# Kernel optimization log

Measured on AMD Instinct MI355X. Metric: run time of the kernel, lower is better.

The kernel has to match this reference:

```python
import jax, jax.numpy as jnp
import numpy as np

NUM_HEADS = 32
NUM_KV_HEADS = 8
HEAD_DIM = 128
ROPE_THETA = 10000.0


def _rope_cos_sin(seq_len, head_dim, dtype):
    # [seq, head_dim/2] angles, duplicated to [seq, head_dim] via concat (rotate-half convention)
    inv_freq = 1.0 / (ROPE_THETA ** (jnp.arange(0, head_dim, 2, dtype=jnp.float32) / head_dim))
    ang = jnp.arange(seq_len, dtype=jnp.float32)[:, None] * inv_freq[None, :]
    ang = jnp.concatenate([ang, ang], axis=-1)
    return jnp.cos(ang).astype(dtype), jnp.sin(ang).astype(dtype)


def _rotate_half(x):
    d = x.shape[-1] // 2
    return jnp.concatenate([-x[..., d:], x[..., :d]], axis=-1)


def setup_inputs() -> dict:
    key = jax.random.key(0)
    ks = jax.random.split(key, 5)
    E = NUM_HEADS * HEAD_DIM
    KVE = NUM_KV_HEADS * HEAD_DIM
    B, S = 2, 2048
    sc_in = 1.0 / np.sqrt(E)
    return {
        "x": jax.random.normal(ks[0], (B, S, E), jnp.float32),
        "Wq": jax.random.normal(ks[1], (E, E), jnp.float32) * sc_in,
        "Wk": jax.random.normal(ks[2], (E, KVE), jnp.float32) * sc_in,
        "Wv": jax.random.normal(ks[3], (E, KVE), jnp.float32) * sc_in,
        "Wo": jax.random.normal(ks[4], (E, E), jnp.float32) * sc_in,
    }


def reference(x, Wq, Wk, Wv, Wo):
    b, s, e = x.shape
    H, KV, D = NUM_HEADS, NUM_KV_HEADS, HEAD_DIM
    G = H // KV
    scale = 1.0 / np.sqrt(D)

    q = (x @ Wq).reshape(b, s, H, D).transpose(0, 2, 1, 3)    # [b,H,s,D]
    k = (x @ Wk).reshape(b, s, KV, D).transpose(0, 2, 1, 3)   # [b,KV,s,D]
    v = (x @ Wv).reshape(b, s, KV, D).transpose(0, 2, 1, 3)   # [b,KV,s,D]

    cos, sin = _rope_cos_sin(s, D, q.dtype)                   # [s,D]
    q = q * cos + _rotate_half(q) * sin
    k = k * cos + _rotate_half(k) * sin

    # GQA: group q heads by kv head instead of repeat_interleaving k/v
    qg = q.reshape(b, KV, G, s, D)
    attn = jnp.einsum("bkgqd,bkvd->bkgqv", qg, k) * scale     # [b,KV,G,s,s]

    causal = jnp.where(
        jnp.arange(s)[:, None] >= jnp.arange(s)[None, :], 0.0, -jnp.inf
    ).astype(jnp.float32)
    attn = attn.astype(jnp.float32) + causal
    attn = jax.nn.softmax(attn, axis=-1).astype(q.dtype)

    out = jnp.einsum("bkgqv,bkvd->bkgqd", attn, v)            # [b,KV,G,s,D]
    out = out.reshape(b, H, s, D).transpose(0, 2, 1, 3).reshape(b, s, H * D)
    return out @ Wo
```

## Files before the change

kernel.cpp:

```cpp
#include <hip/hip_runtime.h>
#include <stdint.h>
#include <math.h>

typedef short bf16x8 __attribute__((ext_vector_type(8)));
typedef float f32x4 __attribute__((ext_vector_type(4)));

#if __has_builtin(__builtin_amdgcn_exp2f)
#define EXP2F(x) __builtin_amdgcn_exp2f(x)
#else
#define EXP2F(x) exp2f(x)
#endif

static constexpr int Bn   = 2;
static constexpr int Sn   = 2048;
static constexpr int NH   = 32;
static constexpr int NKV  = 8;
static constexpr int Dh   = 128;
static constexpr int En   = NH * Dh;
static constexpr int KVEn = NKV * Dh;
static constexpr int QKVE = En + 2 * KVEn;
static constexpr int MT   = Bn * Sn;
static constexpr int QT   = Sn / 128;

__device__ __forceinline__ unsigned short f2bf(float f) {
  unsigned int u = __float_as_uint(f);
  u += 0x7FFFu + ((u >> 16) & 1u);
  return (unsigned short)(u >> 16);
}
__device__ __forceinline__ float bf2f(unsigned short h) {
  return __uint_as_float(((unsigned int)h) << 16);
}

typedef __attribute__((address_space(1))) void* gas_t;
typedef __attribute__((address_space(3))) void* las_t;
__device__ __forceinline__ void gl_lds16(const void* g, void* l) {
  __builtin_amdgcn_global_load_lds((gas_t)(uintptr_t)g, (las_t)(uint32_t)(uintptr_t)l,
                                   16, 0, 0);
}


__global__ void cast_bf16_kernel(const float* __restrict__ x,
                                 unsigned short* __restrict__ y, int n4) {
  int i = blockIdx.x * 256 + threadIdx.x;
  if (i >= n4) return;
  float4 v = ((const float4*)x)[i];
  ushort4 o;
  o.x = f2bf(v.x); o.y = f2bf(v.y); o.z = f2bf(v.z); o.w = f2bf(v.w);
  ((ushort4*)y)[i] = o;
}

__global__ void tcast_kernel(const float* __restrict__ W,
                             unsigned short* __restrict__ WT, int R, int C) {
  __shared__ float t[32][33];
  int tx = threadIdx.x, ty = threadIdx.y;
  int c = blockIdx.x * 32 + tx, r = blockIdx.y * 32 + ty;
  t[ty][tx] = W[(size_t)r * C + c];
  __syncthreads();
  int ro = blockIdx.x * 32 + ty, co = blockIdx.y * 32 + tx;
  WT[(size_t)ro * R + co] = f2bf(t[tx][ty]);
}

__global__ void rope_table_kernel(float2* __restrict__ cs) {
  int i = blockIdx.x * 256 + threadIdx.x;
  int s = i >> 6, d = i & 63;
  float inv = powf(10000.0f, -(float)d * (1.0f / 64.0f));
  float a = (float)s * inv;
  cs[i] = make_float2(cosf(a), sinf(a));
}

__global__ void rope_kernel(unsigned short* __restrict__ q,
                            const float2* __restrict__ cs, int rowstride, float scl) {
  int row = blockIdx.x;
  int s = row & (Sn - 1);
  int hl = threadIdx.x >> 6, d = threadIdx.x & 63;
  int h = blockIdx.y * 4 + hl;
  size_t base = (size_t)row * rowstride + (size_t)h * Dh + d;
  float2 c = cs[s * 64 + d];
  float x0 = bf2f(q[base]), x1 = bf2f(q[base + 64]);
  q[base]      = f2bf((x0 * c.x - x1 * c.y) * scl);
  q[base + 64] = f2bf((x1 * c.x + x0 * c.y) * scl);
}

__global__ void vtrans_kernel(const unsigned short* __restrict__ V, int rowstride,
                              unsigned short* __restrict__ Vt) {
  __shared__ unsigned short t[32][33];
  int bk = blockIdx.z;
  int b = bk >> 3, kv = bk & 7;
  int d = blockIdx.x * 32 + threadIdx.x;
  int s = blockIdx.y * 32 + threadIdx.y;
  t[threadIdx.y][threadIdx.x] = V[(size_t)(b * Sn + s) * rowstride + kv * Dh + d];
  __syncthreads();
  int dd = blockIdx.x * 32 + threadIdx.y;
  int so = blockIdx.y * 32 + threadIdx.x;
  Vt[((size_t)bk * Dh + dd) * Sn + so] = t[threadIdx.x][threadIdx.y];
}


__global__ __launch_bounds__(512, 2) void gemm256_kernel(
    const unsigned short* __restrict__ A, const unsigned short* __restrict__ BT,
    void* __restrict__ Cout, int M, int N, int K, int out_f32) {
  __shared__ unsigned short lds[2][4][128 * 64];
  const int tid = threadIdx.x;
  const int lane = tid & 63, wave = tid >> 6;
  const int r15 = lane & 15, kg = lane >> 4;
  const int wm = wave >> 2, wn = wave & 3;
  const int m0 = blockIdx.y * 256, n0 = blockIdx.x * 256;
  const char* Ab = (const char*)A;
  const char* Bb = (const char*)BT;
  const int KT = K >> 6;

  f32x4 acc[8][4] = {};

  auto stage = [&](int ktile, int buf) {
    int k0 = ktile * 64;
#pragma unroll
    for (int half = 0; half < 2; ++half)
#pragma unroll
      for (int ld = 0; ld < 2; ++ld) {
        int f = (ld * 512 + tid) * 16;
        int row = f >> 7, cb = f & 127;
        int scb = cb ^ ((row & 7) << 4);
        gl_lds16(Ab + ((size_t)(m0 + half * 128 + row) * K + k0) * 2 + scb,
                 (char*)lds[buf][half] + f);
        gl_lds16(Bb + ((size_t)(n0 + half * 128 + row) * K + k0) * 2 + scb,
                 (char*)lds[buf][2 + half] + f);
      }
  };

  stage(0, 0);
  stage(1, 1);
  asm volatile("s_waitcnt vmcnt(8)" ::: "memory");
  __builtin_amdgcn_sched_barrier(0);
  __builtin_amdgcn_s_barrier();
  __builtin_amdgcn_sched_barrier(0);

  for (int kt = 0; kt < KT; ++kt) {
    const int cur = kt & 1;
    const char* Abase = (const char*)lds[cur][wm];
    const char* Bbase = (const char*)lds[cur][2 + (wn >> 1)];
    const int brow0 = (wn & 1) * 64;

#pragma unroll
    for (int ks = 0; ks < 2; ++ks) {
      bf16x8 bfr[4];
#pragma unroll
      for (int nf = 0; nf < 4; ++nf) {
        int br = brow0 + nf * 16 + r15;
        bfr[nf] = *(const bf16x8*)(Bbase + br * 128 +
                                   ((ks * 64 + kg * 16) ^ ((br & 7) << 4)));
      }
#pragma unroll
      for (int mh = 0; mh < 2; ++mh) {
        bf16x8 afr[4];
#pragma unroll
        for (int mf = 0; mf < 4; ++mf) {
          int ar = mh * 64 + mf * 16 + r15;
          afr[mf] = *(const bf16x8*)(Abase + ar * 128 +
                                     ((ks * 64 + kg * 16) ^ ((ar & 7) << 4)));
        }
        __builtin_amdgcn_s_setprio(1);
#pragma unroll
        for (int mf = 0; mf < 4; ++mf)
#pragma unroll
          for (int nf = 0; nf < 4; ++nf)
            acc[mh * 4 + mf][nf] = __builtin_amdgcn_mfma_f32_16x16x32_bf16(
                afr[mf], bfr[nf], acc[mh * 4 + mf][nf], 0, 0, 0);
        __builtin_amdgcn_s_setprio(0);
      }
    }

    __builtin_amdgcn_sched_barrier(0);
    __builtin_amdgcn_s_barrier();
    __builtin_amdgcn_sched_barrier(0);
    if (kt + 2 < KT) {
      stage(kt + 2, cur);
      asm volatile("s_waitcnt vmcnt(8)" ::: "memory");
    } else {
      asm volatile("s_waitcnt vmcnt(0)" ::: "memory");
    }
    __builtin_amdgcn_sched_barrier(0);
    __builtin_amdgcn_s_barrier();
    __builtin_amdgcn_sched_barrier(0);
  }

#pragma unroll
  for (int mh = 0; mh < 2; ++mh)
#pragma unroll
    for (int mf = 0; mf < 4; ++mf)
#pragma unroll
      for (int nf = 0; nf < 4; ++nf)
#pragma unroll
        for (int t = 0; t < 4; ++t) {
          int row = m0 + wm * 128 + mh * 64 + mf * 16 + kg * 4 + t;
          int col = n0 + wn * 64 + nf * 16 + r15;
          if (out_f32)
            ((float*)Cout)[(size_t)row * N + col] = acc[mh * 4 + mf][nf][t];
          else
            ((unsigned short*)Cout)[(size_t)row * N + col] = f2bf(acc[mh * 4 + mf][nf][t]);
        }
}


__device__ __forceinline__ void sm_update(f32x4 sc[4], f32x4 o[8],
                                          float mrow[4], float lrow[4],
                                          bool diag, int qrow0, int kt,
                                          int r15, int kg, char* Pw) {
  if (diag) {
#pragma unroll
    for (int kf = 0; kf < 4; ++kf) {
      int kvg = kt * 64 + kf * 16 + r15;
#pragma unroll
      for (int t = 0; t < 4; ++t)
        if (kvg > qrow0 + kg * 4 + t) sc[kf][t] = -1e30f;
    }
  }
  float mx[4], sm[4];
#pragma unroll
  for (int t = 0; t < 4; ++t) {
    float v = fmaxf(fmaxf(sc[0][t], sc[1][t]), fmaxf(sc[2][t], sc[3][t]));
#pragma unroll
    for (int off = 1; off < 16; off <<= 1) v = fmaxf(v, __shfl_xor(v, off, 16));
    mx[t] = fmaxf(mrow[t], v);
    sm[t] = EXP2F(mrow[t] - mx[t]);
    mrow[t] = mx[t];
  }
#pragma unroll
  for (int kf = 0; kf < 4; ++kf)
#pragma unroll
    for (int t = 0; t < 4; ++t) sc[kf][t] = EXP2F(sc[kf][t] - mx[t]);
#pragma unroll
  for (int t = 0; t < 4; ++t) {
    float v = sc[0][t] + sc[1][t] + sc[2][t] + sc[3][t];
#pragma unroll
    for (int off = 1; off < 16; off <<= 1) v += __shfl_xor(v, off, 16);
    lrow[t] = lrow[t] * sm[t] + v;
  }
#pragma unroll
  for (int nf = 0; nf < 8; ++nf)
#pragma unroll
    for (int t = 0; t < 4; ++t) o[nf][t] *= sm[t];
#pragma unroll
  for (int kf = 0; kf < 4; ++kf)
#pragma unroll
    for (int t = 0; t < 4; ++t) {
      int r = kg * 4 + t, c = kf * 16 + r15;
      *(unsigned short*)(Pw + r * 128 + ((c * 2) ^ ((r & 7) << 4))) = f2bf(sc[kf][t]);
    }
}

__global__ __launch_bounds__(512, 4) void attn_kernel(
    const unsigned short* __restrict__ Q, const unsigned short* __restrict__ Kl,
    const unsigned short* __restrict__ Vt, unsigned short* __restrict__ AO) {
  __shared__ unsigned short Ks[2][64 * 128];
  __shared__ unsigned short Vs[2][128 * 64];
  __shared__ unsigned short Ps[8][16 * 64];
  const int tid = threadIdx.x, lane = tid & 63, wave = tid >> 6;
  const int h = blockIdx.x, b = blockIdx.z;
  const int qt = (QT - 1) - blockIdx.y;
  const int kvh = h >> 2;
  const int r15 = lane & 15, kg = lane >> 4;
  const int qrow0 = qt * 128 + wave * 16;
  const int kmax = 2 * qt + 2;

  bf16x8 qf[4];
#pragma unroll
  for (int db = 0; db < 4; ++db)
    qf[db] = *(const bf16x8*)&Q[(size_t)(b * Sn + qrow0 + r15) * QKVE +
                                h * Dh + db * 32 + kg * 8];

  f32x4 o[8] = {};
  float mrow[4] = {-1e30f, -1e30f, -1e30f, -1e30f};
  float lrow[4] = {0.f, 0.f, 0.f, 0.f};

  const char* Kbase = (const char*)Kl + (size_t)(b * Sn) * (QKVE * 2) + kvh * 256;
  const char* Vbase = (const char*)Vt + (size_t)((b * NKV + kvh) * Dh) * (Sn * 2);

  auto stage = [&](int kt, int bi) {
#pragma unroll
    for (int c = 0; c < 2; ++c) {
      int f = (c * 512 + tid) * 16;
      int row = f >> 8, cb = f & 255;
      gl_lds16(Kbase + (size_t)(kt * 64 + row) * (QKVE * 2) + (cb ^ ((row & 7) << 4)),
               (char*)Ks[bi] + f);
    }
#pragma unroll
    for (int c = 0; c < 2; ++c) {
      int f = (c * 512 + tid) * 16;
      int row = f >> 7, cb = f & 127;
      gl_lds16(Vbase + (size_t)row * (Sn * 2) + kt * 128 + (cb ^ ((row & 7) << 4)),
               (char*)Vs[bi] + f);
    }
  };

  stage(0, 0);
  __syncthreads();

  for (int kt = 0; kt < kmax; ++kt) {
    const int cur = kt & 1;
    if (kt + 1 < kmax) stage(kt + 1, cur ^ 1);
    if (kt * 64 <= qrow0 + 15) {
      const char* Kc = (const char*)Ks[cur];
      const char* Vc = (const char*)Vs[cur];
      f32x4 sc[4] = {};
      __builtin_amdgcn_s_setprio(1);
#pragma unroll
      for (int db = 0; db < 4; ++db) {
#pragma unroll
        for (int kf = 0; kf < 4; ++kf) {
          int krow = kf * 16 + r15;
          int cb = (db * 32 + kg * 8) * 2;
          bf16x8 kb = *(const bf16x8*)(Kc + krow * 256 + (cb ^ ((krow & 7) << 4)));
          sc[kf] = __builtin_amdgcn_mfma_f32_16x16x32_bf16(qf[db], kb, sc[kf], 0, 0, 0);
        }
      }
      __builtin_amdgcn_s_setprio(0);

      char* Pw = (char*)Ps[wave];
      bool diag = (kt * 64 + 63) > qrow0;
      sm_update(sc, o, mrow, lrow, diag, qrow0, kt, r15, kg, Pw);

      __builtin_amdgcn_s_setprio(1);
#pragma unroll
      for (int ks = 0; ks < 2; ++ks) {
        bf16x8 pa = *(const bf16x8*)(Pw + r15 * 128 + ((kg * 16 + ks * 64) ^ ((r15 & 7) << 4)));
#pragma unroll
        for (int nf = 0; nf < 8; ++nf) {
          int vrow = nf * 16 + r15;
          int cb = (ks * 32 + kg * 8) * 2;
          bf16x8 vb = *(const bf16x8*)(Vc + vrow * 128 + (cb ^ ((vrow & 7) << 4)));
          o[nf] = __builtin_amdgcn_mfma_f32_16x16x32_bf16(pa, vb, o[nf], 0, 0, 0);
        }
      }
      __builtin_amdgcn_s_setprio(0);
    }
    __syncthreads();
  }

  float rinv[4];
#pragma unroll
  for (int t = 0; t < 4; ++t) rinv[t] = 1.0f / lrow[t];
#pragma unroll
  for (int nf = 0; nf < 8; ++nf)
#pragma unroll
    for (int t = 0; t < 4; ++t) {
      int srow = qrow0 + kg * 4 + t;
      AO[(size_t)(b * Sn + srow) * En + h * Dh + nf * 16 + r15] = f2bf(o[nf][t] * rinv[t]);
    }
}


extern "C" void kernel_launch(void* const* d_in, const int* in_sizes, int n_in,
                              void* d_out, int out_size, void* d_ws, size_t ws_size,
                              hipStream_t stream) {
  const float* x  = (const float*)d_in[0];
  const float* Wq = (const float*)d_in[1];
  const float* Wk = (const float*)d_in[2];
  const float* Wv = (const float*)d_in[3];
  const float* Wo = (const float*)d_in[4];

  char* ws = (char*)d_ws;
  size_t off = 0;
  auto alloc = [&](size_t bytes) -> char* {
    char* p = ws + off;
    off += (bytes + 255) & ~(size_t)255;
    return p;
  };
  unsigned short* xb   = (unsigned short*)alloc((size_t)MT * En * 2);
  unsigned short* Wqkv = (unsigned short*)alloc((size_t)QKVE * En * 2);
  unsigned short* WoT  = (unsigned short*)alloc((size_t)En * En * 2);
  unsigned short* Cqkv = (unsigned short*)alloc((size_t)MT * QKVE * 2);
  unsigned short* Vt   = (unsigned short*)alloc((size_t)MT * KVEn * 2);
  float2* cs           = (float2*)alloc((size_t)Sn * 64 * sizeof(float2));
  unsigned short* AO   = xb;

  cast_bf16_kernel<<<MT * (En / 4) / 256, 256, 0, stream>>>(x, xb, MT * En / 4);
  tcast_kernel<<<dim3(En / 32, En / 32), dim3(32, 32), 0, stream>>>(Wq, Wqkv, En, En);
  tcast_kernel<<<dim3(KVEn / 32, En / 32), dim3(32, 32), 0, stream>>>(
      Wk, Wqkv + (size_t)En * En, En, KVEn);
  tcast_kernel<<<dim3(KVEn / 32, En / 32), dim3(32, 32), 0, stream>>>(
      Wv, Wqkv + (size_t)(En + KVEn) * En, En, KVEn);
  tcast_kernel<<<dim3(En / 32, En / 32), dim3(32, 32), 0, stream>>>(Wo, WoT, En, En);
  rope_table_kernel<<<Sn * 64 / 256, 256, 0, stream>>>(cs);

  gemm256_kernel<<<dim3(QKVE / 256, MT / 256), 512, 0, stream>>>(
      xb, Wqkv, Cqkv, MT, QKVE, En, 0);

  const float scl = 0.08838834764831845f * 1.4426950408889634f;
  rope_kernel<<<dim3(MT, NH / 4), 256, 0, stream>>>(Cqkv, cs, QKVE, scl);
  rope_kernel<<<dim3(MT, NKV / 4), 256, 0, stream>>>(Cqkv + En, cs, QKVE, 1.0f);
  vtrans_kernel<<<dim3(Dh / 32, Sn / 32, Bn * NKV), dim3(32, 32), 0, stream>>>(
      Cqkv + En + KVEn, QKVE, Vt);

  attn_kernel<<<dim3(NH, QT, Bn), 512, 0, stream>>>(Cqkv, Cqkv + En, Vt, AO);

  gemm256_kernel<<<dim3(En / 256, MT / 256), 512, 0, stream>>>(
      AO, WoT, d_out, MT, En, En, 1);
}
```

Baseline: 619.8 us.

## Restructure bf16 GEMM into 8-phase ping-pong schedule with per-quadrant staging

Rewrites the 256x256 GEMM main loop as eight phases per pair of K-tiles. Each phase computes one 128x128 quadrant (mh, nh) and issues the global-to-LDS load of one half-tile, so that loads and MFMA work are interleaved at finer granularity. The warp-to-output mapping changes from a 2x4 layout with 128x64 per wave to 64x32 sub-blocks repeated in each quadrant, and A and B fragments are reused across phases. This adds more barriers and hand-tuned vmcnt waits, and it assumes KT is even and at least 4.

```diff
diff --git a/kernel.cpp b/kernel.cpp
--- a/kernel.cpp
+++ b/kernel.cpp
@@ -37,6 +37,11 @@
   __builtin_amdgcn_global_load_lds((gas_t)(uintptr_t)g, (las_t)(uint32_t)(uintptr_t)l,
                                    16, 0, 0);
 }
+
+#define VMW(n)  asm volatile("s_waitcnt vmcnt(" #n ")" ::: "memory")
+#define LGKM0   asm volatile("s_waitcnt lgkmcnt(0)" ::: "memory")
+#define SCHEDB  __builtin_amdgcn_sched_barrier(0)
+#define BAR     __builtin_amdgcn_s_barrier()
 
 
 __global__ void cast_bf16_kernel(const float* __restrict__ x,
@@ -103,101 +108,119 @@
   const int tid = threadIdx.x;
   const int lane = tid & 63, wave = tid >> 6;
   const int r15 = lane & 15, kg = lane >> 4;
-  const int wm = wave >> 2, wn = wave & 3;
+  const int wr = wave >> 2, wc = wave & 3;
   const int m0 = blockIdx.y * 256, n0 = blockIdx.x * 256;
   const char* Ab = (const char*)A;
   const char* Bb = (const char*)BT;
   const int KT = K >> 6;
 
-  f32x4 acc[8][4] = {};
-
-  auto stage = [&](int ktile, int buf) {
-    int k0 = ktile * 64;
-#pragma unroll
-    for (int half = 0; half < 2; ++half)
-#pragma unroll
-      for (int ld = 0; ld < 2; ++ld) {
-        int f = (ld * 512 + tid) * 16;
-        int row = f >> 7, cb = f & 127;
-        int scb = cb ^ ((row & 7) << 4);
-        gl_lds16(Ab + ((size_t)(m0 + half * 128 + row) * K + k0) * 2 + scb,
-                 (char*)lds[buf][half] + f);
-        gl_lds16(Bb + ((size_t)(n0 + half * 128 + row) * K + k0) * 2 + scb,
-                 (char*)lds[buf][2 + half] + f);
-      }
-  };
-
-  stage(0, 0);
-  stage(1, 1);
-  asm volatile("s_waitcnt vmcnt(8)" ::: "memory");
-  __builtin_amdgcn_sched_barrier(0);
-  __builtin_amdgcn_s_barrier();
-  __builtin_amdgcn_sched_barrier(0);
-
-  for (int kt = 0; kt < KT; ++kt) {
-    const int cur = kt & 1;
-    const char* Abase = (const char*)lds[cur][wm];
-    const char* Bbase = (const char*)lds[cur][2 + (wn >> 1)];
-    const int brow0 = (wn & 1) * 64;
-
-#pragma unroll
-    for (int ks = 0; ks < 2; ++ks) {
-      bf16x8 bfr[4];
-#pragma unroll
-      for (int nf = 0; nf < 4; ++nf) {
-        int br = brow0 + nf * 16 + r15;
-        bfr[nf] = *(const bf16x8*)(Bbase + br * 128 +
-                                   ((ks * 64 + kg * 16) ^ ((br & 7) << 4)));
-      }
-#pragma unroll
-      for (int mh = 0; mh < 2; ++mh) {
-        bf16x8 afr[4];
-#pragma unroll
-        for (int mf = 0; mf < 4; ++mf) {
-          int ar = mh * 64 + mf * 16 + r15;
-          afr[mf] = *(const bf16x8*)(Abase + ar * 128 +
-                                     ((ks * 64 + kg * 16) ^ ((ar & 7) << 4)));
-        }
-        __builtin_amdgcn_s_setprio(1);
-#pragma unroll
-        for (int mf = 0; mf < 4; ++mf)
-#pragma unroll
-          for (int nf = 0; nf < 4; ++nf)
-            acc[mh * 4 + mf][nf] = __builtin_amdgcn_mfma_f32_16x16x32_bf16(
-                afr[mf], bfr[nf], acc[mh * 4 + mf][nf], 0, 0, 0);
-        __builtin_amdgcn_s_setprio(0);
-      }
-    }
-
-    __builtin_amdgcn_sched_barrier(0);
-    __builtin_amdgcn_s_barrier();
-    __builtin_amdgcn_sched_barrier(0);
-    if (kt + 2 < KT) {
-      stage(kt + 2, cur);
-      asm volatile("s_waitcnt vmcnt(8)" ::: "memory");
-    } else {
-      asm volatile("s_waitcnt vmcnt(0)" ::: "memory");
-    }
-    __builtin_amdgcn_sched_barrier(0);
-    __builtin_amdgcn_s_barrier();
-    __builtin_amdgcn_sched_barrier(0);
+  f32x4 acc[2][2][4][2] = {};
+  bf16x8 ar[4][2];
+  bf16x8 br[2][2][2];
+
+#define STAGE_H(SRC, ROW0, KT_, SLOT)                                         \
+  do {                                                                        \
+    _Pragma("unroll") for (int ld = 0; ld < 2; ++ld) {                        \
+      int _f = (ld * 512 + tid) * 16;                                         \
+      int _row = _f >> 7, _cb = _f & 127;                                     \
+      gl_lds16(SRC + ((size_t)((ROW0) + _row) * K + (KT_) * 64) * 2 +         \
+                   (_cb ^ ((_row & 7) << 4)),                                 \
+               (char*)(SLOT) + _f);                                           \
+    }                                                                         \
+  } while (0)
+
+#define GPHASE(MH, NH, BUF, DO_LDA, DO_LDB, STAGE_STMT, WAIT_STMT)            \
+  do {                                                                        \
+    if (DO_LDA) {                                                             \
+      const char* _as = (const char*)lds[BUF][MH];                            \
+      _Pragma("unroll") for (int mf = 0; mf < 4; ++mf) {                      \
+        int _r = wr * 64 + mf * 16 + r15;                                     \
+        int _sw = (_r & 7) << 4;                                              \
+        ar[mf][0] = *(const bf16x8*)(_as + _r * 128 + ((kg * 16) ^ _sw));     \
+        ar[mf][1] = *(const bf16x8*)(_as + _r * 128 + ((64 + kg * 16) ^ _sw));\
+      }                                                                       \
+    }                                                                         \
+    if (DO_LDB) {                                                             \
+      const char* _bs = (const char*)lds[BUF][2 + NH];                        \
+      _Pragma("unroll") for (int nf = 0; nf < 2; ++nf) {                      \
+        int _r = wc * 32 + nf * 16 + r15;                                     \
+        int _sw = (_r & 7) << 4;                                              \
+        br[NH][nf][0] =                                                       \
+            *(const bf16x8*)(_bs + _r * 128 + ((kg * 16) ^ _sw));             \
+        br[NH][nf][1] =                                                       \
+            *(const bf16x8*)(_bs + _r * 128 + ((64 + kg * 16) ^ _sw));        \
+      }                                                                       \
+    }                                                                         \
+    STAGE_STMT;                                                               \
+    BAR;                                                                      \
+    if ((DO_LDA) || (DO_LDB)) { LGKM0; }                                      \
+    SCHEDB;                                                                   \
+    __builtin_amdgcn_s_setprio(1);                                            \
+    _Pragma("unroll") for (int mf = 0; mf < 4; ++mf)                          \
+      _Pragma("unroll") for (int nf = 0; nf < 2; ++nf) {                      \
+        acc[MH][NH][mf][nf] = __builtin_amdgcn_mfma_f32_16x16x32_bf16(        \
+            ar[mf][0], br[NH][nf][0], acc[MH][NH][mf][nf], 0, 0, 0);          \
+        acc[MH][NH][mf][nf] = __builtin_amdgcn_mfma_f32_16x16x32_bf16(        \
+            ar[mf][1], br[NH][nf][1], acc[MH][NH][mf][nf], 0, 0, 0);          \
+      }                                                                       \
+    __builtin_amdgcn_s_setprio(0);                                            \
+    SCHEDB;                                                                   \
+    WAIT_STMT;                                                                \
+    BAR;                                                                      \
+    SCHEDB;                                                                   \
+  } while (0)
+
+  STAGE_H(Ab, m0,       0, lds[0][0]);
+  STAGE_H(Bb, n0,       0, lds[0][2]);
+  STAGE_H(Ab, m0 + 128, 0, lds[0][1]);
+  STAGE_H(Bb, n0 + 128, 0, lds[0][3]);
+  STAGE_H(Ab, m0,       1, lds[1][0]);
+  STAGE_H(Bb, n0,       1, lds[1][2]);
+  VMW(8);
+  SCHEDB;
+  BAR;
+  SCHEDB;
+
+  for (int k = 0; k + 2 < KT; k += 2) {
+    GPHASE(0, 0, 0, true,  true,  STAGE_H(Ab, m0 + 128, k + 1, lds[1][1]), VMW(6));
+    GPHASE(0, 1, 0, false, true,  STAGE_H(Bb, n0 + 128, k + 1, lds[1][3]), VMW(10));
+    GPHASE(1, 0, 0, true,  false, STAGE_H(Ab, m0,       k + 2, lds[0][0]), (void)0);
+    GPHASE(1, 1, 0, false, false, STAGE_H(Bb, n0,       k + 2, lds[0][2]), VMW(8));
+    GPHASE(0, 0, 1, true,  true,  STAGE_H(Ab, m0 + 128, k + 2, lds[0][1]), VMW(6));
+    GPHASE(0, 1, 1, false, true,  STAGE_H(Bb, n0 + 128, k + 2, lds[0][3]), VMW(10));
+    GPHASE(1, 0, 1, true,  false, STAGE_H(Ab, m0,       k + 3, lds[1][0]), (void)0);
+    GPHASE(1, 1, 1, false, false, STAGE_H(Bb, n0,       k + 3, lds[1][2]), VMW(8));
   }
+  GPHASE(0, 0, 0, true,  true,  STAGE_H(Ab, m0 + 128, KT - 1, lds[1][1]), VMW(6));
+  GPHASE(0, 1, 0, false, true,  STAGE_H(Bb, n0 + 128, KT - 1, lds[1][3]), VMW(10));
+  GPHASE(1, 0, 0, true,  false, (void)0, (void)0);
+  GPHASE(1, 1, 0, false, false, (void)0, VMW(0));
+  GPHASE(0, 0, 1, true,  true,  (void)0, (void)0);
+  GPHASE(0, 1, 1, false, true,  (void)0, (void)0);
+  GPHASE(1, 0, 1, true,  false, (void)0, (void)0);
+  GPHASE(1, 1, 1, false, false, (void)0, (void)0);
+
+#undef GPHASE
+#undef STAGE_H
 
 #pragma unroll
   for (int mh = 0; mh < 2; ++mh)
 #pragma unroll
-    for (int mf = 0; mf < 4; ++mf)
-#pragma unroll
-      for (int nf = 0; nf < 4; ++nf)
-#pragma unroll
-        for (int t = 0; t < 4; ++t) {
-          int row = m0 + wm * 128 + mh * 64 + mf * 16 + kg * 4 + t;
-          int col = n0 + wn * 64 + nf * 16 + r15;
-          if (out_f32)
-            ((float*)Cout)[(size_t)row * N + col] = acc[mh * 4 + mf][nf][t];
-          else
-            ((unsigned short*)Cout)[(size_t)row * N + col] = f2bf(acc[mh * 4 + mf][nf][t]);
-        }
+    for (int nh = 0; nh < 2; ++nh)
+#pragma unroll
+      for (int mf = 0; mf < 4; ++mf)
+#pragma unroll
+        for (int nf = 0; nf < 2; ++nf)
+#pragma unroll
+          for (int t = 0; t < 4; ++t) {
+            int row = m0 + mh * 128 + wr * 64 + mf * 16 + kg * 4 + t;
+            int col = n0 + nh * 128 + wc * 32 + nf * 16 + r15;
+            if (out_f32)
+              ((float*)Cout)[(size_t)row * N + col] = acc[mh][nh][mf][nf][t];
+            else
+              ((unsigned short*)Cout)[(size_t)row * N + col] =
+                  f2bf(acc[mh][nh][mf][nf][t]);
+          }
 }
 
 
```

New measurement: 617.9 us. Within noise of the previous version (-0.3%).
